# Kernel optimization log

Hardware: AMD Instinct MI355X
Metric: run time of the kernel (lower is better)

## Reference

```python
import jax, jax.numpy as jnp
import numpy as np

SEGMENT_LENGTHS = [2048, 4096, 8192]
DILATION_RATES = [1, 2, 4]
BATCH, SEQ_LEN, HEADS, HEAD_DIM = 1, 8192, 16, 64
SCALE = HEAD_DIM ** (-0.5)


def _hilbert_index_to_xy(index, n):
    # Exact replica of the torch module's integer Hilbert d->(x,y) mapping.
    x = y = 0
    s = 1
    while s < n:
        rx = 1 & (index // 2)
        ry = 1 & (index ^ rx)
        if ry == 0:
            if rx == 1:
                x, y = s - 1 - y, s - 1 - x
            x, y = y, x
        x += s * rx
        y += s * ry
        index //= 4
        s *= 2
    return x, y


def _hilbert_perm(n):
    # Replicates _generate_hilbert_indices, including the fill-in tail and
    d = 1
    while d * d < n:
        d *= 2
    idx = []
    for i in range(min(n, d * d)):
        x, y = _hilbert_index_to_xy(i, d)
        p = x * d + y
        if p < n:
            idx.append(p)
    if len(idx) < n:
        idx.extend(range(len(idx), n))
    perm = np.array(idx[:n], dtype=np.int64)
    inv = np.zeros(n, dtype=np.int64)
    inv[perm] = np.arange(n, dtype=np.int64)
    return perm, inv


_PERM_CACHE = {}


def _get_perm(n):
    if n not in _PERM_CACHE:
        _PERM_CACHE[n] = _hilbert_perm(n)
    return _PERM_CACHE[n]


def setup_inputs() -> dict:
    key = jax.random.key(0)
    kq, kk, kv = jax.random.split(key, 3)
    shape = (BATCH, SEQ_LEN, HEADS, HEAD_DIM)
    return {
        "q": jax.random.normal(kq, shape, dtype=jnp.float32),
        "k": jax.random.normal(kk, shape, dtype=jnp.float32),
        "v": jax.random.normal(kv, shape, dtype=jnp.float32),
    }


def reference(q, k, v) -> jnp.ndarray:
    B, L, H, D = q.shape
    n_groups = len(SEGMENT_LENGTHS)
    heads_per_group = max(1, H // n_groups)
    out = jnp.zeros_like(q)
    for g, (seg_len, dil) in enumerate(zip(SEGMENT_LENGTHS, DILATION_RATES)):
        S = min(seg_len, L)
        h0 = g * heads_per_group
        if h0 >= H:
            continue
        h1 = min(h0 + heads_per_group, H)
        assert L % S == 0, "seq_len must tile into segments"
        N = L // S  # number of segments
        Hg = h1 - h0
        # [B, N, S, Hg, D]
        qg = q[:, :, h0:h1].reshape(B, N, S, Hg, D)
        kg = k[:, :, h0:h1].reshape(B, N, S, Hg, D)
        vg = v[:, :, h0:h1].reshape(B, N, S, Hg, D)
        if S > 64:
            perm, inv = _get_perm(S)
        else:
            perm = np.arange(S, dtype=np.int64)
            inv = perm
        # dilation applied AFTER Hilbert ordering -> compose the gathers
        kv_idx = perm[np.arange(0, S, dil)]
        qp = qg[:, :, perm]           # [B,N,S,Hg,D]
        kd = kg[:, :, kv_idx]         # [B,N,S/dil,Hg,D]
        vd = vg[:, :, kv_idx]
        scores = jnp.einsum('bnqhd,bnkhd->bnhqk', qp, kd) * SCALE
        attn = jnp.nan_to_num(jax.nn.softmax(scores, axis=-1))
        og = jnp.einsum('bnhqk,bnkhd->bnqhd', attn, vd)  # [B,N,S,Hg,D]
        og = og[:, :, inv]            # inverse Hilbert scatter
        out = out.at[:, :, h0:h1].set(og.reshape(B, L, Hg, D))
    return out
```

## Files before the change

### kernel.cpp

```cpp
#include <hip/hip_runtime.h>
#include <hip/hip_bf16.h>

typedef __attribute__((ext_vector_type(8))) short bf16x8;
typedef __attribute__((ext_vector_type(4))) short s16x4;
typedef __attribute__((ext_vector_type(4))) float f32x4;
typedef __attribute__((ext_vector_type(4))) unsigned u32x4;

#define LDK 72

__device__ __forceinline__ short f2b(float f) {
    union { float f; unsigned u; } c; c.f = f;
    unsigned r = c.u + 0x7fffu + ((c.u >> 16) & 1u);
    return (short)(r >> 16);
}
__device__ __forceinline__ unsigned pack2(float a, float b) {
    return (unsigned)(unsigned short)f2b(a) | ((unsigned)(unsigned short)f2b(b) << 16);
}

__device__ inline int hilbert_p(int index, int d) {
    int x = 0, y = 0;
    for (int s = 1; s < d; s <<= 1) {
        int rx = (index >> 1) & 1;
        int ry = (index ^ rx) & 1;
        if (ry == 0) {
            if (rx == 1) {
                int nx = s - 1 - y;
                int ny = s - 1 - x;
                x = nx; y = ny;
            }
            int t = x; x = y; y = t;
        }
        x += s * rx;
        y += s * ry;
        index >>= 2;
    }
    return x * d + y;
}

__global__ void setup_kv(int* __restrict__ kv) {
    int t = blockIdx.x * blockDim.x + threadIdx.x;
    if (t >= 3 * 2048) return;
    int g = t >> 11;
    int j = t & 2047;
    int p;
    if (g == 0)      p = j;
    else if (g == 1) p = hilbert_p(2 * j, 64);
    else             p = hilbert_p(4 * j, 128);
    kv[t] = p;
}

__global__ void zero_h15(float* __restrict__ out) {
    int idx = blockIdx.x * blockDim.x + threadIdx.x;
    int l = idx >> 4;
    int c = idx & 15;
    ((float4*)out)[(l * 16 + 15) * 16 + c] = make_float4(0.f, 0.f, 0.f, 0.f);
}

__global__ __launch_bounds__(256, 4) void attn_kernel(
    const float* __restrict__ Q, const float* __restrict__ K,
    const float* __restrict__ V, float* __restrict__ O,
    const int* __restrict__ kvlist)
{
    __shared__ short lds_k [64 * LDK];
    __shared__ short lds_vt[64 * LDK];
    __shared__ short lds_p [128 * LDK];

    const int bx = blockIdx.x;
    const int g  = bx / 320;
    const int r  = bx - g * 320;
    const int hl = r >> 6;
    const int qb = r & 63;

    const int S      = 2048 << g;
    const int h      = g * 5 + hl;
    const int qglob  = qb * 128;
    const int segrow = qglob & ~(S - 1);
    const int* kv    = kvlist + g * 2048;

    const int tid  = threadIdx.x;
    const int wave = tid >> 6;
    const int lane = tid & 63;
    const int ln   = lane & 15;
    const int quad = lane >> 4;

    const float cs = 0.125f * 1.44269504088896f;
    bf16x8 qf[2][2];
#pragma unroll
    for (int m2 = 0; m2 < 2; ++m2) {
        int qrow = qglob + wave * 32 + m2 * 16 + ln;
        const float* qp = Q + ((size_t)(qrow * 16 + h)) * 64;
#pragma unroll
        for (int kh = 0; kh < 2; ++kh) {
            const float4* p4 = (const float4*)(qp + kh * 32 + quad * 8);
            float4 a = p4[0], b = p4[1];
            bf16x8 f;
            f[0] = f2b(a.x * cs); f[1] = f2b(a.y * cs);
            f[2] = f2b(a.z * cs); f[3] = f2b(a.w * cs);
            f[4] = f2b(b.x * cs); f[5] = f2b(b.y * cs);
            f[6] = f2b(b.z * cs); f[7] = f2b(b.w * cs);
            qf[m2][kh] = f;
        }
    }

    f32x4 oacc[2][4];
#pragma unroll
    for (int a = 0; a < 2; ++a)
#pragma unroll
        for (int b = 0; b < 4; ++b)
            oacc[a][b] = (f32x4){0.f, 0.f, 0.f, 0.f};
    float lp[2] = {0.f, 0.f};

    const int j  = tid >> 2;
    const int c  = tid & 3;
    const int d0 = c << 4;
    const int jr = (j + 16 * c) & 63;

    for (int kt = 0; kt < 32; ++kt) {
        __syncthreads();
        {
            int p = kv[kt * 64 + j];
            size_t off = ((size_t)((segrow + p) * 16 + h)) * 64 + d0;
            const float4* kp4 = (const float4*)(K + off);
            const float4* vp4 = (const float4*)(V + off);
            float4 ka = kp4[0], kb = kp4[1], kc = kp4[2], kd = kp4[3];
            unsigned* dst = (unsigned*)&lds_k[j * LDK + d0];
            *((u32x4*)dst)       = (u32x4){pack2(ka.x, ka.y), pack2(ka.z, ka.w),
                                           pack2(kb.x, kb.y), pack2(kb.z, kb.w)};
            *((u32x4*)(dst + 4)) = (u32x4){pack2(kc.x, kc.y), pack2(kc.z, kc.w),
                                           pack2(kd.x, kd.y), pack2(kd.z, kd.w)};
            float4 va = vp4[0], vb = vp4[1], vc = vp4[2], vd = vp4[3];
            short* vt = &lds_vt[d0 * LDK + jr];
            vt[0*LDK]  = f2b(va.x); vt[1*LDK]  = f2b(va.y);
            vt[2*LDK]  = f2b(va.z); vt[3*LDK]  = f2b(va.w);
            vt[4*LDK]  = f2b(vb.x); vt[5*LDK]  = f2b(vb.y);
            vt[6*LDK]  = f2b(vb.z); vt[7*LDK]  = f2b(vb.w);
            vt[8*LDK]  = f2b(vc.x); vt[9*LDK]  = f2b(vc.y);
            vt[10*LDK] = f2b(vc.z); vt[11*LDK] = f2b(vc.w);
            vt[12*LDK] = f2b(vd.x); vt[13*LDK] = f2b(vd.y);
            vt[14*LDK] = f2b(vd.z); vt[15*LDK] = f2b(vd.w);
        }
        __syncthreads();

        bf16x8 kf[4][2];
#pragma unroll
        for (int kg = 0; kg < 4; ++kg)
#pragma unroll
            for (int kh = 0; kh < 2; ++kh)
                kf[kg][kh] = *(const bf16x8*)&lds_k[(kg * 16 + ln) * LDK + kh * 32 + quad * 8];

#pragma unroll
        for (int m2 = 0; m2 < 2; ++m2) {
            float lacc = 0.f;
#pragma unroll
            for (int kg = 0; kg < 4; ++kg) {
                f32x4 st = (f32x4){0.f, 0.f, 0.f, 0.f};
                st = __builtin_amdgcn_mfma_f32_16x16x32_bf16(kf[kg][0], qf[m2][0], st, 0, 0, 0);
                st = __builtin_amdgcn_mfma_f32_16x16x32_bf16(kf[kg][1], qf[m2][1], st, 0, 0, 0);
                float p0 = __builtin_amdgcn_exp2f(st[0]);
                float p1 = __builtin_amdgcn_exp2f(st[1]);
                float p2 = __builtin_amdgcn_exp2f(st[2]);
                float p3 = __builtin_amdgcn_exp2f(st[3]);
                lacc += (p0 + p1) + (p2 + p3);
                s16x4 pk = (s16x4){f2b(p0), f2b(p1), f2b(p2), f2b(p3)};
                *(s16x4*)&lds_p[(wave * 32 + m2 * 16 + ln) * LDK + kg * 16 + quad * 4] = pk;
            }
            lp[m2] += lacc;
        }
        __syncthreads();

        bf16x8 vf[4][2];
#pragma unroll
        for (int n4 = 0; n4 < 4; ++n4)
#pragma unroll
            for (int kh = 0; kh < 2; ++kh) {
                int bk = (kh * 32 + quad * 8 + 16 * n4) & 63;
                vf[n4][kh] = *(const bf16x8*)&lds_vt[(n4 * 16 + ln) * LDK + bk];
            }
#pragma unroll
        for (int m2 = 0; m2 < 2; ++m2) {
            const short* prow = &lds_p[(wave * 32 + m2 * 16 + ln) * LDK];
            bf16x8 ap0 = *(const bf16x8*)(prow + quad * 8);
            bf16x8 ap1 = *(const bf16x8*)(prow + 32 + quad * 8);
#pragma unroll
            for (int n4 = 0; n4 < 4; ++n4) {
                oacc[m2][n4] = __builtin_amdgcn_mfma_f32_16x16x32_bf16(ap0, vf[n4][0], oacc[m2][n4], 0, 0, 0);
                oacc[m2][n4] = __builtin_amdgcn_mfma_f32_16x16x32_bf16(ap1, vf[n4][1], oacc[m2][n4], 0, 0, 0);
            }
        }
    }

    lp[0] += __shfl_xor(lp[0], 16, 64);
    lp[0] += __shfl_xor(lp[0], 32, 64);
    lp[1] += __shfl_xor(lp[1], 16, 64);
    lp[1] += __shfl_xor(lp[1], 32, 64);

#pragma unroll
    for (int m2 = 0; m2 < 2; ++m2) {
#pragma unroll
        for (int rg = 0; rg < 4; ++rg) {
            float lv  = __shfl(lp[m2], quad * 4 + rg, 64);
            float inv = 1.0f / lv;
            int qrow = qglob + wave * 32 + m2 * 16 + quad * 4 + rg;
            float* op = O + ((size_t)(qrow * 16 + h)) * 64;
#pragma unroll
            for (int n4 = 0; n4 < 4; ++n4)
                op[n4 * 16 + ln] = oacc[m2][n4][rg] * inv;
        }
    }
}

extern "C" void kernel_launch(void* const* d_in, const int* in_sizes, int n_in,
                              void* d_out, int out_size, void* d_ws, size_t ws_size,
                              hipStream_t stream) {
    const float* q = (const float*)d_in[0];
    const float* k = (const float*)d_in[1];
    const float* v = (const float*)d_in[2];
    float* out = (float*)d_out;
    int* kv = (int*)d_ws;

    setup_kv<<<24, 256, 0, stream>>>(kv);
    zero_h15<<<512, 256, 0, stream>>>(out);
    attn_kernel<<<960, 256, 0, stream>>>(q, k, v, out, kv);
}
```

Measured before the change: 247.8 us.

## Pre-gather K/V into swizzled bf16 tiles and stream them via global_load_lds

A new pre-pass kernel gathers the Hilbert/dilated K and V rows once, converts them to bf16, transposes V, and writes them into XOR-swizzled 64x64 tiles in workspace. The attention kernel then copies each tile straight into LDS with global_load_lds, so the fp32 gather and conversion are no longer repeated by every query block that shares a segment. The zeroing of head 15 moves into the attention kernel and the index setup kernel is removed. The cost is an extra kernel launch and a workspace round-trip, and the workspace must be large enough for both bf16 tile buffers.

```diff
diff --git a/kernel.cpp b/kernel.cpp
--- a/kernel.cpp
+++ b/kernel.cpp
@@ -4,17 +4,19 @@
 typedef __attribute__((ext_vector_type(8))) short bf16x8;
 typedef __attribute__((ext_vector_type(4))) short s16x4;
 typedef __attribute__((ext_vector_type(4))) float f32x4;
-typedef __attribute__((ext_vector_type(4))) unsigned u32x4;
-
-#define LDK 72
-
-__device__ __forceinline__ short f2b(float f) {
-    union { float f; unsigned u; } c; c.f = f;
-    unsigned r = c.u + 0x7fffu + ((c.u >> 16) & 1u);
-    return (short)(r >> 16);
-}
-__device__ __forceinline__ unsigned pack2(float a, float b) {
-    return (unsigned)(unsigned short)f2b(a) | ((unsigned)(unsigned short)f2b(b) << 16);
+
+#define LDKP 72
+
+__device__ __forceinline__ unsigned pk2(float a, float b) {
+    union { __hip_bfloat162 h2; unsigned u; } c;
+    c.h2 = __float22bfloat162_rn(make_float2(a, b));
+    return c.u;
+}
+
+__device__ __forceinline__ void gld16(const void* g, void* l) {
+    __builtin_amdgcn_global_load_lds(
+        (const __attribute__((address_space(1))) unsigned*)g,
+        (__attribute__((address_space(3))) unsigned*)l, 16, 0, 0);
 }
 
 __device__ inline int hilbert_p(int index, int d) {
@@ -37,45 +39,75 @@
     return x * d + y;
 }
 
-__global__ void setup_kv(int* __restrict__ kv) {
-    int t = blockIdx.x * blockDim.x + threadIdx.x;
-    if (t >= 3 * 2048) return;
-    int g = t >> 11;
-    int j = t & 2047;
-    int p;
-    if (g == 0)      p = j;
-    else if (g == 1) p = hilbert_p(2 * j, 64);
-    else             p = hilbert_p(4 * j, 128);
-    kv[t] = p;
-}
-
-__global__ void zero_h15(float* __restrict__ out) {
-    int idx = blockIdx.x * blockDim.x + threadIdx.x;
-    int l = idx >> 4;
-    int c = idx & 15;
-    ((float4*)out)[(l * 16 + 15) * 16 + c] = make_float4(0.f, 0.f, 0.f, 0.f);
+__global__ __launch_bounds__(256) void gather_kv(
+    const float* __restrict__ K, const float* __restrict__ V,
+    short* __restrict__ Kp, short* __restrict__ Vp)
+{
+    __shared__ short vt[64 * LDKP];
+
+    const int b = blockIdx.x;
+    int g, rb;
+    if (b < 640)      { g = 0; rb = b; }
+    else if (b < 960) { g = 1; rb = b - 640; }
+    else              { g = 2; rb = b - 960; }
+    const int nseg   = 4 >> g;
+    const int hl     = rb / (nseg * 32);
+    const int r2     = rb - hl * (nseg * 32);
+    const int seg    = r2 >> 5;
+    const int kt     = r2 & 31;
+    const int h      = g * 5 + hl;
+    const int S      = 2048 << g;
+    const int segrow = seg * S;
+    const int dgrid  = (g == 2) ? 128 : 64;
+    const size_t tile_s = (size_t)b * 4096;
+
+    for (int it = threadIdx.x; it < 512; it += 256) {
+        const int j  = it >> 3;
+        const int c8 = it & 7;
+        const int ii = kt * 64 + j;
+        const int p  = (g == 0) ? ii : hilbert_p(ii << g, dgrid);
+        const size_t src = ((size_t)((segrow + p) * 16 + h)) * 64 + c8 * 8;
+        const float4* kp = (const float4*)(K + src);
+        const float4* vp = (const float4*)(V + src);
+        float4 k0 = kp[0], k1 = kp[1];
+        float4 v0 = vp[0], v1 = vp[1];
+        union { unsigned u[4]; bf16x8 v; } ck, cv;
+        ck.u[0] = pk2(k0.x, k0.y); ck.u[1] = pk2(k0.z, k0.w);
+        ck.u[2] = pk2(k1.x, k1.y); ck.u[3] = pk2(k1.z, k1.w);
+        cv.u[0] = pk2(v0.x, v0.y); cv.u[1] = pk2(v0.z, v0.w);
+        cv.u[2] = pk2(v1.x, v1.y); cv.u[3] = pk2(v1.z, v1.w);
+        *(bf16x8*)&Kp[tile_s + j * 64 + ((c8 ^ (j & 7)) * 8)] = ck.v;
+        *(bf16x8*)&vt[j * LDKP + c8 * 8] = cv.v;
+    }
+    __syncthreads();
+    for (int it = threadIdx.x; it < 512; it += 256) {
+        const int dd = it >> 3;
+        const int k8 = it & 7;
+        union { short s[8]; bf16x8 v; } o;
+#pragma unroll
+        for (int u = 0; u < 8; ++u)
+            o.s[u] = vt[(k8 * 8 + u) * LDKP + dd];
+        *(bf16x8*)&Vp[tile_s + dd * 64 + ((k8 ^ (dd & 7)) * 8)] = o.v;
+    }
 }
 
 __global__ __launch_bounds__(256, 4) void attn_kernel(
-    const float* __restrict__ Q, const float* __restrict__ K,
-    const float* __restrict__ V, float* __restrict__ O,
-    const int* __restrict__ kvlist)
+    const float* __restrict__ Q, float* __restrict__ O,
+    const short* __restrict__ Kp, const short* __restrict__ Vp)
 {
-    __shared__ short lds_k [64 * LDK];
-    __shared__ short lds_vt[64 * LDK];
-    __shared__ short lds_p [128 * LDK];
+    __shared__ __align__(16) short ldsK[4096];
+    __shared__ __align__(16) short ldsV[4096];
+    __shared__ __align__(16) short ldsP[128 * LDKP];
 
     const int bx = blockIdx.x;
     const int g  = bx / 320;
     const int r  = bx - g * 320;
     const int hl = r >> 6;
     const int qb = r & 63;
-
-    const int S      = 2048 << g;
-    const int h      = g * 5 + hl;
-    const int qglob  = qb * 128;
-    const int segrow = qglob & ~(S - 1);
-    const int* kv    = kvlist + g * 2048;
+    const int h  = g * 5 + hl;
+    const int qglob = qb * 128;
+    const int seg   = qb >> (4 + g);
+    const int tile0 = ((g == 0) ? 0 : (g == 1) ? 640 : 960) + (hl * (4 >> g) + seg) * 32;
 
     const int tid  = threadIdx.x;
     const int wave = tid >> 6;
@@ -83,6 +115,14 @@
     const int ln   = lane & 15;
     const int quad = lane >> 4;
 
+    if (g == 0 && hl == 0) {
+        const float4 z = make_float4(0.f, 0.f, 0.f, 0.f);
+        for (int i = tid; i < 2048; i += 256) {
+            int row = qglob + (i >> 4);
+            ((float4*)O)[(size_t)(row * 16 + 15) * 16 + (i & 15)] = z;
+        }
+    }
+
     const float cs = 0.125f * 1.44269504088896f;
     bf16x8 qf[2][2];
 #pragma unroll
@@ -93,12 +133,10 @@
         for (int kh = 0; kh < 2; ++kh) {
             const float4* p4 = (const float4*)(qp + kh * 32 + quad * 8);
             float4 a = p4[0], b = p4[1];
-            bf16x8 f;
-            f[0] = f2b(a.x * cs); f[1] = f2b(a.y * cs);
-            f[2] = f2b(a.z * cs); f[3] = f2b(a.w * cs);
-            f[4] = f2b(b.x * cs); f[5] = f2b(b.y * cs);
-            f[6] = f2b(b.z * cs); f[7] = f2b(b.w * cs);
-            qf[m2][kh] = f;
+            union { unsigned u[4]; bf16x8 v; } f;
+            f.u[0] = pk2(a.x * cs, a.y * cs); f.u[1] = pk2(a.z * cs, a.w * cs);
+            f.u[2] = pk2(b.x * cs, b.y * cs); f.u[3] = pk2(b.z * cs, b.w * cs);
+            qf[m2][kh] = f.v;
         }
     }
 
@@ -110,34 +148,18 @@
             oacc[a][b] = (f32x4){0.f, 0.f, 0.f, 0.f};
     float lp[2] = {0.f, 0.f};
 
-    const int j  = tid >> 2;
-    const int c  = tid & 3;
-    const int d0 = c << 4;
-    const int jr = (j + 16 * c) & 63;
-
     for (int kt = 0; kt < 32; ++kt) {
         __syncthreads();
         {
-            int p = kv[kt * 64 + j];
-            size_t off = ((size_t)((segrow + p) * 16 + h)) * 64 + d0;
-            const float4* kp4 = (const float4*)(K + off);
-            const float4* vp4 = (const float4*)(V + off);
-            float4 ka = kp4[0], kb = kp4[1], kc = kp4[2], kd = kp4[3];
-            unsigned* dst = (unsigned*)&lds_k[j * LDK + d0];
-            *((u32x4*)dst)       = (u32x4){pack2(ka.x, ka.y), pack2(ka.z, ka.w),
-                                           pack2(kb.x, kb.y), pack2(kb.z, kb.w)};
-            *((u32x4*)(dst + 4)) = (u32x4){pack2(kc.x, kc.y), pack2(kc.z, kc.w),
-                                           pack2(kd.x, kd.y), pack2(kd.z, kd.w)};
-            float4 va = vp4[0], vb = vp4[1], vc = vp4[2], vd = vp4[3];
-            short* vt = &lds_vt[d0 * LDK + jr];
-            vt[0*LDK]  = f2b(va.x); vt[1*LDK]  = f2b(va.y);
-            vt[2*LDK]  = f2b(va.z); vt[3*LDK]  = f2b(va.w);
-            vt[4*LDK]  = f2b(vb.x); vt[5*LDK]  = f2b(vb.y);
-            vt[6*LDK]  = f2b(vb.z); vt[7*LDK]  = f2b(vb.w);
-            vt[8*LDK]  = f2b(vc.x); vt[9*LDK]  = f2b(vc.y);
-            vt[10*LDK] = f2b(vc.z); vt[11*LDK] = f2b(vc.w);
-            vt[12*LDK] = f2b(vd.x); vt[13*LDK] = f2b(vd.y);
-            vt[14*LDK] = f2b(vd.z); vt[15*LDK] = f2b(vd.w);
+            const size_t tb = (size_t)(tile0 + kt) << 13;
+            const char* kgp = (const char*)Kp + tb + (wave << 11) + (lane << 4);
+            const char* vgp = (const char*)Vp + tb + (wave << 11) + (lane << 4);
+            char* klp = (char*)ldsK + (wave << 11);
+            char* vlp = (char*)ldsV + (wave << 11);
+            gld16(kgp,        klp);
+            gld16(kgp + 1024, klp + 1024);
+            gld16(vgp,        vlp);
+            gld16(vgp + 1024, vlp + 1024);
         }
         __syncthreads();
 
@@ -146,7 +168,7 @@
         for (int kg = 0; kg < 4; ++kg)
 #pragma unroll
             for (int kh = 0; kh < 2; ++kh)
-                kf[kg][kh] = *(const bf16x8*)&lds_k[(kg * 16 + ln) * LDK + kh * 32 + quad * 8];
+                kf[kg][kh] = *(const bf16x8*)&ldsK[(kg * 16 + ln) * 64 + (((kh * 4 + quad) ^ (ln & 7)) * 8)];
 
 #pragma unroll
         for (int m2 = 0; m2 < 2; ++m2) {
@@ -161,8 +183,9 @@
                 float p2 = __builtin_amdgcn_exp2f(st[2]);
                 float p3 = __builtin_amdgcn_exp2f(st[3]);
                 lacc += (p0 + p1) + (p2 + p3);
-                s16x4 pk = (s16x4){f2b(p0), f2b(p1), f2b(p2), f2b(p3)};
-                *(s16x4*)&lds_p[(wave * 32 + m2 * 16 + ln) * LDK + kg * 16 + quad * 4] = pk;
+                union { unsigned u[2]; s16x4 s; } pc;
+                pc.u[0] = pk2(p0, p1); pc.u[1] = pk2(p2, p3);
+                *(s16x4*)&ldsP[(wave * 32 + m2 * 16 + ln) * LDKP + kg * 16 + quad * 4] = pc.s;
             }
             lp[m2] += lacc;
         }
@@ -172,13 +195,11 @@
 #pragma unroll
         for (int n4 = 0; n4 < 4; ++n4)
 #pragma unroll
-            for (int kh = 0; kh < 2; ++kh) {
-                int bk = (kh * 32 + quad * 8 + 16 * n4) & 63;
-                vf[n4][kh] = *(const bf16x8*)&lds_vt[(n4 * 16 + ln) * LDK + bk];
-            }
+            for (int kh = 0; kh < 2; ++kh)
+                vf[n4][kh] = *(const bf16x8*)&ldsV[(n4 * 16 + ln) * 64 + (((kh * 4 + quad) ^ (ln & 7)) * 8)];
 #pragma unroll
         for (int m2 = 0; m2 < 2; ++m2) {
-            const short* prow = &lds_p[(wave * 32 + m2 * 16 + ln) * LDK];
+            const short* prow = &ldsP[(wave * 32 + m2 * 16 + ln) * LDKP];
             bf16x8 ap0 = *(const bf16x8*)(prow + quad * 8);
             bf16x8 ap1 = *(const bf16x8*)(prow + 32 + quad * 8);
 #pragma unroll
@@ -216,9 +237,9 @@
     const float* k = (const float*)d_in[1];
     const float* v = (const float*)d_in[2];
     float* out = (float*)d_out;
-    int* kv = (int*)d_ws;
-
-    setup_kv<<<24, 256, 0, stream>>>(kv);
-    zero_h15<<<512, 256, 0, stream>>>(out);
-    attn_kernel<<<960, 256, 0, stream>>>(q, k, v, out, kv);
-}
+    short* Kp = (short*)d_ws;
+    short* Vp = Kp + (size_t)1120 * 4096;
+
+    gather_kv<<<1120, 256, 0, stream>>>(k, v, Kp, Vp);
+    attn_kernel<<<960, 256, 0, stream>>>(q, out, Kp, Vp);
+}
```

After: 206.2 us. -16.8%, faster.
